# Performance work log

Measured on AMD Instinct MI355X. Metric: run time of the kernel, lower is better.

The kernel has to match this reference:

```python
import jax, jax.numpy as jnp
import numpy as np

KK = 10.0  # sigmoid sharpness constant `kk` from the source

def sigmoid_k(x):
    return jax.nn.sigmoid(KK * x)

def setup_inputs() -> dict:
    key = jax.random.key(0)
    k1, k2, k3 = jax.random.split(key, 3)
    B, L = 8192, 4096
    # contiguous valid-prefix padding mask with random per-row lengths in [L//4, L)
    lens = jax.random.randint(k1, (B,), L // 4, L)
    mask = (jnp.arange(L)[None, :] < lens[:, None]).astype(jnp.float32)
    t = jax.random.uniform(k2, (B, 1), dtype=jnp.float32) * L          # crop centers
    l = 1.0 + jax.random.uniform(k3, (B, 1), dtype=jnp.float32) * (L / 2.0)  # half-widths
    return {"t": t, "l": l, "mask": mask, "length": L}

def reference(t, l, mask, length):
    t = t.reshape(-1, 1)
    l = l.reshape(-1, 1)
    # boundaries of the valid region (replaces the CPU numpy argmax round-trip)
    left = (jnp.argmax(mask, axis=-1).astype(jnp.float32) - 1.0)[:, None]          # [B,1]
    right = (float(length) - jnp.argmax(mask[:, ::-1], axis=-1).astype(jnp.float32))[:, None]  # [B,1]
    sentence_length = jnp.sum(mask, axis=-1, keepdims=True) / 2.0                   # [B,1]
    l_eff = jnp.where(l <= sentence_length, sentence_length, l)
    t_left = (t - l_eff) * (t - l_eff >= left).astype(jnp.float32)
    t_left = jnp.where(t_left == 0.0, left, t_left)
    t_right = ((t + l_eff) <= right).astype(jnp.float32) * (t + l_eff)
    t_right = jnp.where(t_right == 0.0, right, t_right)
    pos = jnp.arange(length, dtype=jnp.float32)                                     # [L]
    crop_mask = sigmoid_k(pos - t_left) - sigmoid_k(pos - t_right)                  # [B,L]
    crop_mask = (crop_mask >= 0.5).astype(jnp.float32) * mask
    return crop_mask
```

## Files before the change

kernel.cpp:

```cpp
#include <hip/hip_runtime.h>
#include <hip/hip_bf16.h>
#include <climits>


#define BLOCK 256
#define NVMAX 8

__device__ __forceinline__ float sigmoid10(float x) {
    return 1.0f / (1.0f + expf(-10.0f * x));
}

__global__ __launch_bounds__(BLOCK) void attention_crop_kernel(
    const float* __restrict__ t, const float* __restrict__ l,
    const float* __restrict__ mask, float* __restrict__ out, int Llen) {
    const int row = blockIdx.x;
    const int tid = threadIdx.x;
    const int nvec = Llen >> 2;

    const float4* mrow = (const float4*)(mask + (size_t)row * Llen);
    float4* orow = (float4*)(out + (size_t)row * Llen);

    float4 mv[NVMAX];
    float lsum = 0.0f;
    int lmin = INT_MAX;
    int lmax = -1;
    #pragma unroll
    for (int i = 0; i < NVMAX; ++i) {
        const int j = tid + i * BLOCK;
        if (j < nvec) {
            float4 m = mrow[j];
            mv[i] = m;
            const int e = j << 2;
            lsum += m.x + m.y + m.z + m.w;
            if (m.x > 0.5f) { lmin = min(lmin, e);     lmax = max(lmax, e);     }
            if (m.y > 0.5f) { lmin = min(lmin, e + 1); lmax = max(lmax, e + 1); }
            if (m.z > 0.5f) { lmin = min(lmin, e + 2); lmax = max(lmax, e + 2); }
            if (m.w > 0.5f) { lmin = min(lmin, e + 3); lmax = max(lmax, e + 3); }
        }
    }

    #pragma unroll
    for (int off = 32; off > 0; off >>= 1) {
        lsum += __shfl_down(lsum, off);
        lmin = min(lmin, __shfl_down(lmin, off));
        lmax = max(lmax, __shfl_down(lmax, off));
    }

    __shared__ float s_sum[BLOCK / 64];
    __shared__ int s_min[BLOCK / 64], s_max[BLOCK / 64];
    __shared__ float s_tl, s_tr;
    const int lane = tid & 63, wid = tid >> 6;
    if (lane == 0) { s_sum[wid] = lsum; s_min[wid] = lmin; s_max[wid] = lmax; }
    __syncthreads();

    if (tid == 0) {
        float sum = 0.0f; int mn = INT_MAX, mx = -1;
        #pragma unroll
        for (int w = 0; w < BLOCK / 64; ++w) {
            sum += s_sum[w];
            mn = min(mn, s_min[w]);
            mx = max(mx, s_max[w]);
        }
        const int first_one = (mn == INT_MAX) ? 0 : mn;
        const int last_one  = (mx < 0) ? (Llen - 1) : mx;
        const float leftf  = (float)first_one - 1.0f;
        const float rightf = (float)(last_one + 1);
        const float sl = sum * 0.5f;
        const float tv = t[row], lv = l[row];
        const float leff = (lv <= sl) ? sl : lv;
        float tl0 = tv - leff;
        float t_left = (tl0 >= leftf) ? tl0 : 0.0f;
        if (t_left == 0.0f) t_left = leftf;
        float tr0 = tv + leff;
        float t_right = (tr0 <= rightf) ? tr0 : 0.0f;
        if (t_right == 0.0f) t_right = rightf;
        s_tl = t_left;
        s_tr = t_right;
    }
    __syncthreads();

    const float t_left = s_tl, t_right = s_tr;

    #pragma unroll
    for (int i = 0; i < NVMAX; ++i) {
        const int j = tid + i * BLOCK;
        if (j < nvec) {
            const float p0 = (float)(j << 2);
            const float4 m = mv[i];
            float4 o;
            float v;
            v = sigmoid10(p0 - t_left)        - sigmoid10(p0 - t_right);
            o.x = (v >= 0.5f) ? m.x : 0.0f;
            v = sigmoid10(p0 + 1.0f - t_left) - sigmoid10(p0 + 1.0f - t_right);
            o.y = (v >= 0.5f) ? m.y : 0.0f;
            v = sigmoid10(p0 + 2.0f - t_left) - sigmoid10(p0 + 2.0f - t_right);
            o.z = (v >= 0.5f) ? m.z : 0.0f;
            v = sigmoid10(p0 + 3.0f - t_left) - sigmoid10(p0 + 3.0f - t_right);
            o.w = (v >= 0.5f) ? m.w : 0.0f;
            orow[j] = o;
        }
    }
}

extern "C" void kernel_launch(void* const* d_in, const int* in_sizes, int n_in,
                              void* d_out, int out_size, void* d_ws, size_t ws_size,
                              hipStream_t stream) {
    const float* t    = (const float*)d_in[0];
    const float* l    = (const float*)d_in[1];
    const float* mask = (const float*)d_in[2];
    float* out = (float*)d_out;

    const int B = in_sizes[0];
    const int Llen = in_sizes[2] / B;

    attention_crop_kernel<<<B, BLOCK, 0, stream>>>(t, l, mask, out, Llen);
}
```

Measured before the change: 242.7 us.

## Replace per-element sigmoid crop test with closed-form integer interval bounds

Thread 0 of each row now solves analytically for where the difference of two sigmoids crosses 0.5, using a quadratic in exp space. It then refines the resulting integer bounds with a few exact sigmoid evaluations. Every other thread only does two integer compares per element instead of eight expf calls per float4. This removes per-element transcendental work, at the cost of a serial computation on one thread per row and some risk of boundary mismatches where float rounding differs from the reference.

```diff
diff --git a/kernel.cpp b/kernel.cpp
--- a/kernel.cpp
+++ b/kernel.cpp
@@ -8,6 +8,9 @@
 
 __device__ __forceinline__ float sigmoid10(float x) {
     return 1.0f / (1.0f + expf(-10.0f * x));
+}
+__device__ __forceinline__ float fdiff(float p, float tl, float tr) {
+    return sigmoid10(p - tl) - sigmoid10(p - tr);
 }
 
 __global__ __launch_bounds__(BLOCK) void attention_crop_kernel(
@@ -22,8 +25,7 @@
 
     float4 mv[NVMAX];
     float lsum = 0.0f;
-    int lmin = INT_MAX;
-    int lmax = -1;
+    int lmin = INT_MAX, lmax = -1;
     #pragma unroll
     for (int i = 0; i < NVMAX; ++i) {
         const int j = tid + i * BLOCK;
@@ -48,7 +50,7 @@
 
     __shared__ float s_sum[BLOCK / 64];
     __shared__ int s_min[BLOCK / 64], s_max[BLOCK / 64];
-    __shared__ float s_tl, s_tr;
+    __shared__ int s_lo, s_hi;
     const int lane = tid & 63, wid = tid >> 6;
     if (lane == 0) { s_sum[wid] = lsum; s_min[wid] = lmin; s_max[wid] = lmax; }
     __syncthreads();
@@ -74,29 +76,44 @@
         float tr0 = tv + leff;
         float t_right = (tr0 <= rightf) ? tr0 : 0.0f;
         if (t_right == 0.0f) t_right = rightf;
-        s_tl = t_left;
-        s_tr = t_right;
+
+        int lo = 1, hi = 0;
+        const float c = expf(-10.0f * (t_right - t_left));
+        const float b = 1.0f - 3.0f * c;
+        const float disc = b * b - 4.0f * c;
+        if (b > 0.0f && disc >= 0.0f) {
+            const float xp = 0.5f * (b + sqrtf(disc));
+            const float p_lo = t_left - 0.1f * logf(xp);
+            const float p_hi = (t_left + t_right) - p_lo;
+            lo = (int)ceilf(p_lo);
+            hi = (int)floorf(p_hi);
+            #pragma unroll 1
+            for (int k = 0; k < 4 && fdiff((float)(lo - 1), t_left, t_right) >= 0.5f; ++k) --lo;
+            #pragma unroll 1
+            for (int k = 0; k < 4 && fdiff((float)lo, t_left, t_right) < 0.5f; ++k) ++lo;
+            #pragma unroll 1
+            for (int k = 0; k < 4 && fdiff((float)(hi + 1), t_left, t_right) >= 0.5f; ++k) ++hi;
+            #pragma unroll 1
+            for (int k = 0; k < 4 && fdiff((float)hi, t_left, t_right) < 0.5f; ++k) --hi;
+        }
+        s_lo = lo;
+        s_hi = hi;
     }
     __syncthreads();
 
-    const float t_left = s_tl, t_right = s_tr;
+    const int lo = s_lo, hi = s_hi;
 
     #pragma unroll
     for (int i = 0; i < NVMAX; ++i) {
         const int j = tid + i * BLOCK;
         if (j < nvec) {
-            const float p0 = (float)(j << 2);
+            const int e = j << 2;
             const float4 m = mv[i];
             float4 o;
-            float v;
-            v = sigmoid10(p0 - t_left)        - sigmoid10(p0 - t_right);
-            o.x = (v >= 0.5f) ? m.x : 0.0f;
-            v = sigmoid10(p0 + 1.0f - t_left) - sigmoid10(p0 + 1.0f - t_right);
-            o.y = (v >= 0.5f) ? m.y : 0.0f;
-            v = sigmoid10(p0 + 2.0f - t_left) - sigmoid10(p0 + 2.0f - t_right);
-            o.z = (v >= 0.5f) ? m.z : 0.0f;
-            v = sigmoid10(p0 + 3.0f - t_left) - sigmoid10(p0 + 3.0f - t_right);
-            o.w = (v >= 0.5f) ? m.w : 0.0f;
+            o.x = (e     >= lo && e     <= hi) ? m.x : 0.0f;
+            o.y = (e + 1 >= lo && e + 1 <= hi) ? m.y : 0.0f;
+            o.z = (e + 2 >= lo && e + 2 <= hi) ? m.z : 0.0f;
+            o.w = (e + 3 >= lo && e + 3 <= hi) ? m.w : 0.0f;
             orow[j] = o;
         }
     }
```

After: 240.8 us. No clear change (-0.8%).
